# Kernel tuning notes

Measured on AMD Instinct MI355X. Metric: run time of the kernel, lower is better.

The kernel has to match this reference:

```python
import jax, jax.numpy as jnp
import numpy as np
from jax import lax

T = 16384
L = 1024  # num_labels; START = L-2, STOP = L-1
NEG = -10000.0


def setup_inputs() -> dict:
    key = jax.random.key(0)
    k1, k2, k3 = jax.random.split(key, 3)
    pred_logits = jax.random.normal(k1, (T, L), dtype=jnp.float32)
    # gold tags avoid the reserved START (L-2) and STOP (L-1) tags
    ref = jax.random.randint(k2, (T,), 0, L - 2)
    transitions = jax.random.normal(k3, (L, L), dtype=jnp.float32)
    transitions = transitions.at[L - 2, :].set(NEG).at[L - 1, :].set(NEG)
    return {"pred_logits": pred_logits, "ref": ref, "transitions": transitions}


def reference(pred_logits, ref, transitions):
    num_labels = transitions.shape[0]
    START = num_labels - 2
    STOP = num_labels - 1

    # ---- forward algorithm (log-sum-exp recurrence over tags) ----
    init = jnp.full((num_labels,), NEG, dtype=pred_logits.dtype).at[START].set(0.0)

    def step(alpha, feat):
        # new_alpha[j] = logsumexp_i(alpha[i] + transitions[j, i]) + feat[j]
        new_alpha = jax.nn.logsumexp(alpha[None, :] + transitions, axis=1) + feat
        return new_alpha, None

    alpha, _ = lax.scan(step, init, pred_logits)
    forward_score = jax.nn.logsumexp(alpha + transitions[STOP])

    # ---- gold path score ----
    prev = jnp.concatenate([jnp.array([START], dtype=ref.dtype), ref[:-1]])
    trans_score = transitions[ref, prev].sum()
    emit_score = jnp.take_along_axis(pred_logits, ref[:, None], axis=1).sum()
    gold_score = trans_score + emit_score + transitions[STOP, ref[-1]]

    # torch returns shape (1,)
    return (forward_score - gold_score).reshape(1)
```

## Files before the change

kernel.cpp:

```cpp
#include <hip/hip_runtime.h>


#define TT    16384
#define LLAB  1024
#define NEGV  -10000.0
#define BQ    32
#define NCH   512
#define KCH   32
#define NPTY  8
#define AGT   __HIP_MEMORY_SCOPE_AGENT

typedef unsigned long long u64;
typedef unsigned int u32;
typedef unsigned short u16;
typedef _Float16 f16;
typedef _Float16 h2 __attribute__((ext_vector_type(2)));
typedef _Float16 f16x8 __attribute__((ext_vector_type(8)));
typedef float f32x4 __attribute__((ext_vector_type(4)));

__device__ __forceinline__ void pub64(u64* p, u64 v) {
  __hip_atomic_store(p, v, __ATOMIC_RELAXED, AGT);
}
__device__ __forceinline__ u64 ald64(const u64* p) {
  return __hip_atomic_load(p, __ATOMIC_RELAXED, AGT);
}
__device__ __forceinline__ u32 pack2(float a, float b) {
  h2 h = {(f16)a, (f16)b};
  return __builtin_bit_cast(u32, h);
}
__device__ __forceinline__ float f16lo(u32 b) {
  return (float)__builtin_bit_cast(f16, (u16)(b & 0xFFFFu));
}
__device__ __forceinline__ float f16hi(u32 b) {
  return (float)__builtin_bit_cast(f16, (u16)(b >> 16));
}
__device__ __forceinline__ int swz(int c, int w) { return w ^ ((c & 7) << 2); }

__device__ __forceinline__ float max4(u32 a, u32 b) {
  return fmaxf(fmaxf(f16lo(a), f16hi(a)), fmaxf(f16lo(b), f16hi(b)));
}

__global__ __launch_bounds__(256) void crf_gold(const float* __restrict__ pred,
                                                const int* __restrict__ ref,
                                                const float* __restrict__ trans,
                                                float* __restrict__ gold) {
  int t = blockIdx.x * 256 + threadIdx.x;
  int r = ref[t];
  int prev = (t == 0) ? (LLAB - 2) : ref[t - 1];
  float v = trans[(size_t)r * LLAB + prev] + pred[(size_t)t * LLAB + r];
  if (t == TT - 1) v += trans[(size_t)(LLAB - 1) * LLAB + r];
#pragma unroll
  for (int off = 32; off >= 1; off >>= 1) v += __shfl_xor(v, off);
  __shared__ float acc[4];
  if ((threadIdx.x & 63) == 0) acc[threadIdx.x >> 6] = v;
  __syncthreads();
  if (threadIdx.x == 0) atomicAdd(gold, acc[0] + acc[1] + acc[2] + acc[3]);
}

__global__ __launch_bounds__(256) void transpose_k(const float* __restrict__ in,
                                                   float* __restrict__ out) {
  __shared__ float t[32][33];
  int bx = blockIdx.x & 31, by = blockIdx.x >> 5;
  int r0 = by * 32, c0 = bx * 32;
  int lr = threadIdx.x >> 3;
  int lc = threadIdx.x & 7;
  float4 v = *(const float4*)&in[(size_t)(r0 + lr) * LLAB + c0 + 4 * lc];
  t[lr][4 * lc] = v.x; t[lr][4 * lc + 1] = v.y;
  t[lr][4 * lc + 2] = v.z; t[lr][4 * lc + 3] = v.w;
  __syncthreads();
  float4 o = {t[4 * lc][lr], t[4 * lc + 1][lr], t[4 * lc + 2][lr], t[4 * lc + 3][lr]};
  *(float4*)&out[(size_t)(c0 + lr) * LLAB + r0 + 4 * lc] = o;
}

__global__ __launch_bounds__(256, 1) void crf_chunks(
    const float* __restrict__ pred, const float* __restrict__ trans,
    const float* __restrict__ transT, u64* __restrict__ pay,
    u32* __restrict__ fl, float* __restrict__ ybuf,
    float* __restrict__ zbuf, double* __restrict__ tlog) {
  const int tid = threadIdx.x;
  const int wv = tid >> 6, l = tid & 63;
  const int lm = l & 15, lg = l >> 4;
  const int gc = tid >> 3, tp = tid & 7;
  const int b = blockIdx.x;
  const int g = b & 31;
  const int party = b >> 5;
  const bool isFwd = (g < 16);
  const int cbase = (g & 15) * KCH;
  const int c1 = cbase + lm, c2 = cbase + lm + 16;
  const int tb1 = c1 * BQ, tb2 = c2 * BQ;
  const int wb = 128 * party + 32 * wv;

  const float* M = isFwd ? trans : transT;
  f16x8 afrag0[32], afrag1[32];
  {
    const float4* rp0 = (const float4*)&M[(size_t)(wb + lm) * LLAB];
    const float4* rp1 = (const float4*)&M[(size_t)(wb + 16 + lm) * LLAB];
#pragma unroll
    for (int kt = 0; kt < 32; ++kt) {
      float4 a = rp0[8 * kt + 2 * lg], c = rp0[8 * kt + 2 * lg + 1];
      f16x8 f;
      f[0] = (f16)__expf(a.x); f[1] = (f16)__expf(a.y);
      f[2] = (f16)__expf(a.z); f[3] = (f16)__expf(a.w);
      f[4] = (f16)__expf(c.x); f[5] = (f16)__expf(c.y);
      f[6] = (f16)__expf(c.z); f[7] = (f16)__expf(c.w);
      afrag0[kt] = f;
      a = rp1[8 * kt + 2 * lg]; c = rp1[8 * kt + 2 * lg + 1];
      f[0] = (f16)__expf(a.x); f[1] = (f16)__expf(a.y);
      f[2] = (f16)__expf(a.z); f[3] = (f16)__expf(a.w);
      f[4] = (f16)__expf(c.x); f[5] = (f16)__expf(c.y);
      f[6] = (f16)__expf(c.z); f[7] = (f16)__expf(c.w);
      afrag1[kt] = f;
    }
  }

  __shared__ __attribute__((aligned(16))) u32 qs[KCH * 512];
  __shared__ float smax[KCH];

  u64* gp64 = pay + (size_t)g * 16384;
  u32* gfl  = fl + (size_t)g * 512;

  {
    float mm;
    if (isFwd) {
      uint4 ones = {0x3C003C00u, 0x3C003C00u, 0x3C003C00u, 0x3C003C00u};
#pragma unroll
      for (int i = 0; i < 16; ++i)
        *(uint4*)&qs[gc * 512 + swz(gc, 64 * tp + 4 * i)] = ones;
      mm = 1.0f;
    } else {
      int trow = (cbase + gc) * BQ + BQ - 1;
      const float4* pp = (const float4*)&pred[(size_t)trow * LLAB + 128 * tp];
      mm = 0.f;
#pragma unroll
      for (int i = 0; i < 16; ++i) {
        float4 e0 = pp[2 * i], e1 = pp[2 * i + 1];
        float a0 = __expf(e0.x), a1 = __expf(e0.y);
        float a2 = __expf(e0.z), a3 = __expf(e0.w);
        float a4 = __expf(e1.x), a5 = __expf(e1.y);
        float a6 = __expf(e1.z), a7 = __expf(e1.w);
        uint4 w4 = {pack2(a0, a1), pack2(a2, a3), pack2(a4, a5), pack2(a6, a7)};
        *(uint4*)&qs[gc * 512 + swz(gc, 64 * tp + 4 * i)] = w4;
        mm = fmaxf(mm, fmaxf(fmaxf(a0, a1), fmaxf(a2, a3)));
        mm = fmaxf(mm, fmaxf(fmaxf(a4, a5), fmaxf(a6, a7)));
      }
#pragma unroll
      for (int off = 1; off <= 4; off <<= 1) mm = fmaxf(mm, __shfl_xor(mm, off));
    }
    if (tp == 0) smax[gc] = mm;
  }
  __syncthreads();

  float4 fe1a, fe1b, fe2a, fe2b;
  {
    int t1 = isFwd ? tb1 : (tb1 + BQ - 2);
    int t2 = isFwd ? tb2 : (tb2 + BQ - 2);
    fe1a = *(const float4*)&pred[(size_t)t1 * LLAB + wb + 4 * lg];
    fe1b = *(const float4*)&pred[(size_t)t1 * LLAB + wb + 16 + 4 * lg];
    fe2a = *(const float4*)&pred[(size_t)t2 * LLAB + wb + 4 * lg];
    fe2b = *(const float4*)&pred[(size_t)t2 * LLAB + wb + 16 + 4 * lg];
  }

  const float C0 = 13359.727f;
  double up = 1.0;

  for (int s = 0; s < BQ; ++s) {
    const bool lastS = (s == BQ - 1);
    const int ps = s & 1;
    const u32 want = (u32)(s + 1);
    if (tid < KCH) up *= (double)smax[tid];
    const float i1 = 1.0f / (C0 * smax[lm]);
    const float i2 = 1.0f / (C0 * smax[lm + 16]);

    f32x4 a00 = {0.f, 0.f, 0.f, 0.f}, a01 = {0.f, 0.f, 0.f, 0.f};
    f32x4 a10 = {0.f, 0.f, 0.f, 0.f}, a11 = {0.f, 0.f, 0.f, 0.f};
#pragma unroll
    for (int kt = 0; kt < 32; ++kt) {
      f16x8 b1 = __builtin_bit_cast(f16x8,
          *(const uint4*)&qs[lm * 512 + swz(lm, 16 * kt + 4 * lg)]);
      f16x8 b2 = __builtin_bit_cast(f16x8,
          *(const uint4*)&qs[(lm + 16) * 512 + swz(lm + 16, 16 * kt + 4 * lg)]);
      a00 = __builtin_amdgcn_mfma_f32_16x16x32_f16(afrag0[kt], b1, a00, 0, 0, 0);
      a01 = __builtin_amdgcn_mfma_f32_16x16x32_f16(afrag1[kt], b1, a01, 0, 0, 0);
      a10 = __builtin_amdgcn_mfma_f32_16x16x32_f16(afrag0[kt], b2, a10, 0, 0, 0);
      a11 = __builtin_amdgcn_mfma_f32_16x16x32_f16(afrag1[kt], b2, a11, 0, 0, 0);
    }

    float4 n1a = fe1a, n1b = fe1b, n2a = fe2a, n2b = fe2b;
    if (!lastS) {
      int sn = s + 1;
      int t1 = isFwd ? (tb1 + sn) : (tb1 + BQ - 2 - sn);
      int t2 = isFwd ? (tb2 + sn) : (tb2 + BQ - 2 - sn);
      if (t1 < tb1) t1 = tb1;
      if (t2 < tb2) t2 = tb2;
      n1a = *(const float4*)&pred[(size_t)t1 * LLAB + wb + 4 * lg];
      n1b = *(const float4*)&pred[(size_t)t1 * LLAB + wb + 16 + 4 * lg];
      n2a = *(const float4*)&pred[(size_t)t2 * LLAB + wb + 4 * lg];
      n2b = *(const float4*)&pred[(size_t)t2 * LLAB + wb + 16 + 4 * lg];
    }

    const bool fold = isFwd || !lastS;
    float o00[4], o01[4], o10[4], o11[4];
    if (fold) {
      o00[0] = a00[0] * __expf(fe1a.x) * i1; o00[1] = a00[1] * __expf(fe1a.y) * i1;
      o00[2] = a00[2] * __expf(fe1a.z) * i1; o00[3] = a00[3] * __expf(fe1a.w) * i1;
      o01[0] = a01[0] * __expf(fe1b.x) * i1; o01[1] = a01[1] * __expf(fe1b.y) * i1;
      o01[2] = a01[2] * __expf(fe1b.z) * i1; o01[3] = a01[3] * __expf(fe1b.w) * i1;
      o10[0] = a10[0] * __expf(fe2a.x) * i2; o10[1] = a10[1] * __expf(fe2a.y) * i2;
      o10[2] = a10[2] * __expf(fe2a.z) * i2; o10[3] = a10[3] * __expf(fe2a.w) * i2;
      o11[0] = a11[0] * __expf(fe2b.x) * i2; o11[1] = a11[1] * __expf(fe2b.y) * i2;
      o11[2] = a11[2] * __expf(fe2b.z) * i2; o11[3] = a11[3] * __expf(fe2b.w) * i2;
    } else {
#pragma unroll
      for (int r = 0; r < 4; ++r) {
        o00[r] = a00[r] * i1; o01[r] = a01[r] * i1;
        o10[r] = a10[r] * i2; o11[r] = a11[r] * i2;
      }
    }

    if (lastS) {
      float* dst = isFwd ? ybuf : zbuf;
      size_t b1 = (size_t)c1 * LLAB + wb + 4 * lg;
      size_t b2 = (size_t)c2 * LLAB + wb + 4 * lg;
#pragma unroll
      for (int r = 0; r < 4; ++r) {
        dst[b1 + r] = o00[r]; dst[b1 + 16 + r] = o01[r];
        dst[b2 + r] = o10[r]; dst[b2 + 16 + r] = o11[r];
      }
      break;
    }

    {
      u64* op = gp64 + (size_t)ps * 8192 + party * 1024;
      int i64 = lm * 32 + 8 * wv + lg;
      pub64(op + i64,       ((u64)pack2(o00[2], o00[3]) << 32) | pack2(o00[0], o00[1]));
      pub64(op + i64 + 4,   ((u64)pack2(o01[2], o01[3]) << 32) | pack2(o01[0], o01[1]));
      pub64(op + i64 + 512, ((u64)pack2(o10[2], o10[3]) << 32) | pack2(o10[0], o10[1]));
      pub64(op + i64 + 516, ((u64)pack2(o11[2], o11[3]) << 32) | pack2(o11[0], o11[1]));
    }
    __syncthreads();
    if (tid == 0)
      __hip_atomic_store(gfl + ps * 256 + party * 32, want, __ATOMIC_RELAXED, AGT);

    {
      const u32* fp = gfl + ps * 256 + (l & 7) * 32;
      bool done = false;
      do {
        if (!done) done = (__hip_atomic_load(fp, __ATOMIC_RELAXED, AGT) >= want);
      } while (!__all(done));
    }

    {
      u64 gv[8][4];
#pragma unroll
      for (int p2 = 0; p2 < 8; ++p2) {
        const u64* pb = gp64 + (size_t)ps * 8192 + p2 * 1024 + tid * 4;
#pragma unroll
        for (int j = 0; j < 4; ++j) gv[p2][j] = ald64(pb + j);
      }
      float mm = 0.f;
#pragma unroll
      for (int p2 = 0; p2 < 8; ++p2) {
#pragma unroll
        for (int j = 0; j < 4; ++j) {
          u32 lo = (u32)gv[p2][j], hi = (u32)(gv[p2][j] >> 32);
          int W = p2 * 64 + 8 * tp + 2 * j;
          uint2 st = {lo, hi};
          *(uint2*)&qs[gc * 512 + swz(gc, W)] = st;
          mm = fmaxf(mm, max4(lo, hi));
        }
      }
#pragma unroll
      for (int off = 1; off <= 4; off <<= 1) mm = fmaxf(mm, __shfl_xor(mm, off));
      if (tp == 0) smax[gc] = mm;
    }
    __syncthreads();
    fe1a = n1a; fe1b = n1b; fe2a = n2a; fe2b = n2b;
  }

  if (!isFwd && party == 0 && tid < KCH) tlog[cbase + tid] = log(up);
}

__global__ __launch_bounds__(256) void crf_stitch(
    const float* __restrict__ ybuf, const float* __restrict__ zbuf,
    const double* __restrict__ tlog, double* __restrict__ dacc) {
  const int cc = blockIdx.x, tid = threadIdx.x;
  double na = 0.0, sa = 0.0;
  for (int j = tid; j < LLAB; j += 256) {
    double yv = (double)ybuf[(size_t)cc * LLAB + j];
    na += yv;
    double zz = (cc + 1 < NCH) ? (double)zbuf[(size_t)(cc + 1) * LLAB + j] : 1.0;
    sa += zz * yv;
  }
#pragma unroll
  for (int off = 32; off >= 1; off >>= 1) {
    na += __shfl_xor(na, off);
    sa += __shfl_xor(sa, off);
  }
  __shared__ double red[2][4];
  if ((tid & 63) == 0) { red[0][tid >> 6] = na; red[1][tid >> 6] = sa; }
  __syncthreads();
  if (tid == 0) {
    double n = red[0][0] + red[0][1] + red[0][2] + red[0][3];
    double sm = red[1][0] + red[1][1] + red[1][2] + red[1][3];
    const double LC0 = log((double)13359.727f);
    atomicAdd(dacc, log(sm) - log(n) + tlog[cc] + (double)BQ * LC0);
  }
}

__global__ void crf_final(const double* __restrict__ dacc,
                          const float* __restrict__ zbuf,
                          const float* __restrict__ gold,
                          float* __restrict__ out) {
  double s = dacc[0] + log((double)zbuf[LLAB - 2]) + NEGV - (double)gold[0];
  out[0] = (float)s;
}

extern "C" void kernel_launch(void* const* d_in, const int* in_sizes, int n_in,
                              void* d_out, int out_size, void* d_ws, size_t ws_size,
                              hipStream_t stream) {
  const float* pred  = (const float*)d_in[0];
  const int*   ref   = (const int*)d_in[1];
  const float* trans = (const float*)d_in[2];
  float* out = (float*)d_out;

  char* ws = (char*)d_ws;
  double* dacc = (double*)(ws + 0);
  float* gold  = (float*)(ws + 8);
  float* transT = (float*)(ws + 1024);
  size_t off = 1024 + (size_t)LLAB * LLAB * 4;
  u64* pay = (u64*)(ws + off);
  off += (size_t)32 * 2 * NPTY * 1024 * 8;
  u32* fl = (u32*)(ws + off);
  const size_t flbytes = (size_t)32 * 512 * 4;
  off += flbytes;
  float* ybuf = (float*)(ws + off); off += (size_t)NCH * LLAB * 4;
  float* zbuf = (float*)(ws + off); off += (size_t)NCH * LLAB * 4;
  double* tlog = (double*)(ws + off);

  hipMemsetAsync(ws, 0, 256, stream);
  hipMemsetAsync(fl, 0, flbytes, stream);
  transpose_k<<<1024, 256, 0, stream>>>(trans, transT);
  crf_gold<<<64, 256, 0, stream>>>(pred, ref, trans, gold);
  crf_chunks<<<256, 256, 0, stream>>>(pred, trans, transT, pay, fl, ybuf, zbuf, tlog);
  crf_stitch<<<NCH, 256, 0, stream>>>(ybuf, zbuf, tlog, dacc);
  crf_final<<<1, 1, 0, stream>>>(dacc, zbuf, gold, out);
}
```

Measured before the change: 373.2 us.

## Fuse auxiliary kernels into chunk kernel and streamline cross-block exchange

Removes the transpose kernel by loading transposed exp-transitions with strided reads directly in the backward blocks. It folds the gold-score computation into the chunk kernel's tail and merges the final reduction into the stitch kernel via an atomic counter, which also replaces two memsets with one. The per-step exchange now keeps each block's own payload in LDS and skips reloading it, and fetches peers' data with 16-byte system-coherent loads instead of 8-byte atomic loads. The result is fewer launches and less global traffic per step, at the cost of uncoalesced setup reads of the transposed matrix.

```diff
diff --git a/kernel.cpp b/kernel.cpp
--- a/kernel.cpp
+++ b/kernel.cpp
@@ -21,8 +21,11 @@
 __device__ __forceinline__ void pub64(u64* p, u64 v) {
   __hip_atomic_store(p, v, __ATOMIC_RELAXED, AGT);
 }
-__device__ __forceinline__ u64 ald64(const u64* p) {
-  return __hip_atomic_load(p, __ATOMIC_RELAXED, AGT);
+__device__ __forceinline__ uint4 ld16_sc(const u32* p) {
+  uint4 r;
+  asm volatile("global_load_dwordx4 %0, %1, off sc0 sc1"
+               : "=v"(r) : "v"(p) : "memory");
+  return r;
 }
 __device__ __forceinline__ u32 pack2(float a, float b) {
   h2 h = {(f16)a, (f16)b};
@@ -36,51 +39,21 @@
 }
 __device__ __forceinline__ int swz(int c, int w) { return w ^ ((c & 7) << 2); }
 
-__device__ __forceinline__ float max4(u32 a, u32 b) {
-  return fmaxf(fmaxf(f16lo(a), f16hi(a)), fmaxf(f16lo(b), f16hi(b)));
-}
-
-__global__ __launch_bounds__(256) void crf_gold(const float* __restrict__ pred,
-                                                const int* __restrict__ ref,
-                                                const float* __restrict__ trans,
-                                                float* __restrict__ gold) {
-  int t = blockIdx.x * 256 + threadIdx.x;
-  int r = ref[t];
-  int prev = (t == 0) ? (LLAB - 2) : ref[t - 1];
-  float v = trans[(size_t)r * LLAB + prev] + pred[(size_t)t * LLAB + r];
-  if (t == TT - 1) v += trans[(size_t)(LLAB - 1) * LLAB + r];
-#pragma unroll
-  for (int off = 32; off >= 1; off >>= 1) v += __shfl_xor(v, off);
-  __shared__ float acc[4];
-  if ((threadIdx.x & 63) == 0) acc[threadIdx.x >> 6] = v;
-  __syncthreads();
-  if (threadIdx.x == 0) atomicAdd(gold, acc[0] + acc[1] + acc[2] + acc[3]);
-}
-
-__global__ __launch_bounds__(256) void transpose_k(const float* __restrict__ in,
-                                                   float* __restrict__ out) {
-  __shared__ float t[32][33];
-  int bx = blockIdx.x & 31, by = blockIdx.x >> 5;
-  int r0 = by * 32, c0 = bx * 32;
-  int lr = threadIdx.x >> 3;
-  int lc = threadIdx.x & 7;
-  float4 v = *(const float4*)&in[(size_t)(r0 + lr) * LLAB + c0 + 4 * lc];
-  t[lr][4 * lc] = v.x; t[lr][4 * lc + 1] = v.y;
-  t[lr][4 * lc + 2] = v.z; t[lr][4 * lc + 3] = v.w;
-  __syncthreads();
-  float4 o = {t[4 * lc][lr], t[4 * lc + 1][lr], t[4 * lc + 2][lr], t[4 * lc + 3][lr]};
-  *(float4*)&out[(size_t)(c0 + lr) * LLAB + r0 + 4 * lc] = o;
+__device__ __forceinline__ float max8(uint4 v) {
+  float m = fmaxf(fmaxf(f16lo(v.x), f16hi(v.x)), fmaxf(f16lo(v.y), f16hi(v.y)));
+  m = fmaxf(m, fmaxf(f16lo(v.z), f16hi(v.z)));
+  m = fmaxf(m, fmaxf(f16lo(v.w), f16hi(v.w)));
+  return m;
 }
 
 __global__ __launch_bounds__(256, 1) void crf_chunks(
     const float* __restrict__ pred, const float* __restrict__ trans,
-    const float* __restrict__ transT, u64* __restrict__ pay,
-    u32* __restrict__ fl, float* __restrict__ ybuf,
-    float* __restrict__ zbuf, double* __restrict__ tlog) {
+    const int* __restrict__ ref, u32* __restrict__ pay, u32* __restrict__ fl,
+    float* __restrict__ ybuf, float* __restrict__ zbuf,
+    double* __restrict__ tlog, float* __restrict__ gold) {
   const int tid = threadIdx.x;
   const int wv = tid >> 6, l = tid & 63;
   const int lm = l & 15, lg = l >> 4;
-  const int gc = tid >> 3, tp = tid & 7;
   const int b = blockIdx.x;
   const int g = b & 31;
   const int party = b >> 5;
@@ -90,11 +63,10 @@
   const int tb1 = c1 * BQ, tb2 = c2 * BQ;
   const int wb = 128 * party + 32 * wv;
 
-  const float* M = isFwd ? trans : transT;
   f16x8 afrag0[32], afrag1[32];
-  {
-    const float4* rp0 = (const float4*)&M[(size_t)(wb + lm) * LLAB];
-    const float4* rp1 = (const float4*)&M[(size_t)(wb + 16 + lm) * LLAB];
+  if (isFwd) {
+    const float4* rp0 = (const float4*)&trans[(size_t)(wb + lm) * LLAB];
+    const float4* rp1 = (const float4*)&trans[(size_t)(wb + 16 + lm) * LLAB];
 #pragma unroll
     for (int kt = 0; kt < 32; ++kt) {
       float4 a = rp0[8 * kt + 2 * lg], c = rp0[8 * kt + 2 * lg + 1];
@@ -111,15 +83,29 @@
       f[6] = (f16)__expf(c.z); f[7] = (f16)__expf(c.w);
       afrag1[kt] = f;
     }
+  } else {
+    const int c0 = wb + lm, cc1 = wb + 16 + lm;
+#pragma unroll
+    for (int kt = 0; kt < 32; ++kt) {
+      f16x8 f0, f1;
+#pragma unroll
+      for (int j = 0; j < 8; ++j) {
+        int k = 32 * kt + 8 * lg + j;
+        f0[j] = (f16)__expf(trans[(size_t)k * LLAB + c0]);
+        f1[j] = (f16)__expf(trans[(size_t)k * LLAB + cc1]);
+      }
+      afrag0[kt] = f0; afrag1[kt] = f1;
+    }
   }
 
   __shared__ __attribute__((aligned(16))) u32 qs[KCH * 512];
   __shared__ float smax[KCH];
 
-  u64* gp64 = pay + (size_t)g * 16384;
-  u32* gfl  = fl + (size_t)g * 512;
+  u32* gpay = pay + (size_t)g * 32768;
+  u32* gfl  = fl + g * 512;
 
   {
+    const int gc = tid >> 3, tp = tid & 7;
     float mm;
     if (isFwd) {
       uint4 ones = {0x3C003C00u, 0x3C003C00u, 0x3C003C00u, 0x3C003C00u};
@@ -219,27 +205,41 @@
 
     if (lastS) {
       float* dst = isFwd ? ybuf : zbuf;
-      size_t b1 = (size_t)c1 * LLAB + wb + 4 * lg;
-      size_t b2 = (size_t)c2 * LLAB + wb + 4 * lg;
+      size_t bb1 = (size_t)c1 * LLAB + wb + 4 * lg;
+      size_t bb2 = (size_t)c2 * LLAB + wb + 4 * lg;
 #pragma unroll
       for (int r = 0; r < 4; ++r) {
-        dst[b1 + r] = o00[r]; dst[b1 + 16 + r] = o01[r];
-        dst[b2 + r] = o10[r]; dst[b2 + 16 + r] = o11[r];
+        dst[bb1 + r] = o00[r]; dst[bb1 + 16 + r] = o01[r];
+        dst[bb2 + r] = o10[r]; dst[bb2 + 16 + r] = o11[r];
       }
       break;
     }
 
+    const u32 q00 = pack2(o00[0], o00[1]), q01 = pack2(o00[2], o00[3]);
+    const u32 q02 = pack2(o01[0], o01[1]), q03 = pack2(o01[2], o01[3]);
+    const u32 q10 = pack2(o10[0], o10[1]), q11 = pack2(o10[2], o10[3]);
+    const u32 q12 = pack2(o11[0], o11[1]), q13 = pack2(o11[2], o11[3]);
     {
-      u64* op = gp64 + (size_t)ps * 8192 + party * 1024;
+      u64* op = (u64*)(gpay + (size_t)ps * 16384 + party * 2048);
       int i64 = lm * 32 + 8 * wv + lg;
-      pub64(op + i64,       ((u64)pack2(o00[2], o00[3]) << 32) | pack2(o00[0], o00[1]));
-      pub64(op + i64 + 4,   ((u64)pack2(o01[2], o01[3]) << 32) | pack2(o01[0], o01[1]));
-      pub64(op + i64 + 512, ((u64)pack2(o10[2], o10[3]) << 32) | pack2(o10[0], o10[1]));
-      pub64(op + i64 + 516, ((u64)pack2(o11[2], o11[3]) << 32) | pack2(o11[0], o11[1]));
+      pub64(op + i64,       ((u64)q01 << 32) | q00);
+      pub64(op + i64 + 4,   ((u64)q03 << 32) | q02);
+      pub64(op + i64 + 512, ((u64)q11 << 32) | q10);
+      pub64(op + i64 + 516, ((u64)q13 << 32) | q12);
     }
     __syncthreads();
     if (tid == 0)
       __hip_atomic_store(gfl + ps * 256 + party * 32, want, __ATOMIC_RELAXED, AGT);
+
+    {
+      int w = 16 * wv + 2 * lg;
+      uint2 s0 = {q00, q01}, s1 = {q02, q03}, s2 = {q10, q11}, s3 = {q12, q13};
+      *(uint2*)&qs[lm * 512 + swz(lm, party * 64 + w)] = s0;
+      *(uint2*)&qs[lm * 512 + swz(lm, party * 64 + w + 8)] = s1;
+      *(uint2*)&qs[(lm + 16) * 512 + swz(lm + 16, party * 64 + w)] = s2;
+      *(uint2*)&qs[(lm + 16) * 512 + swz(lm + 16, party * 64 + w + 8)] = s3;
+    }
+    __syncthreads();
 
     {
       const u32* fp = gfl + ps * 256 + (l & 7) * 32;
@@ -250,69 +250,96 @@
     }
 
     {
-      u64 gv[8][4];
+      const u32* pb = gpay + (size_t)ps * 16384;
+      const int c = tid >> 3, wbase = 8 * (tid & 7);
+      uint4 gv[16];
 #pragma unroll
       for (int p2 = 0; p2 < 8; ++p2) {
-        const u64* pb = gp64 + (size_t)ps * 8192 + p2 * 1024 + tid * 4;
-#pragma unroll
-        for (int j = 0; j < 4; ++j) gv[p2][j] = ald64(pb + j);
-      }
+        if (p2 != party) {
+          gv[2 * p2]     = ld16_sc(pb + p2 * 2048 + tid * 8);
+          gv[2 * p2 + 1] = ld16_sc(pb + p2 * 2048 + tid * 8 + 4);
+        }
+      }
+      asm volatile("s_waitcnt vmcnt(0)" ::: "memory");
+      __builtin_amdgcn_sched_barrier(0);
       float mm = 0.f;
 #pragma unroll
       for (int p2 = 0; p2 < 8; ++p2) {
-#pragma unroll
-        for (int j = 0; j < 4; ++j) {
-          u32 lo = (u32)gv[p2][j], hi = (u32)(gv[p2][j] >> 32);
-          int W = p2 * 64 + 8 * tp + 2 * j;
-          uint2 st = {lo, hi};
-          *(uint2*)&qs[gc * 512 + swz(gc, W)] = st;
-          mm = fmaxf(mm, max4(lo, hi));
+        uint4 va, vb;
+        if (p2 == party) {
+          va = *(const uint4*)&qs[c * 512 + swz(c, p2 * 64 + wbase)];
+          vb = *(const uint4*)&qs[c * 512 + swz(c, p2 * 64 + wbase + 4)];
+        } else {
+          va = gv[2 * p2]; vb = gv[2 * p2 + 1];
+          *(uint4*)&qs[c * 512 + swz(c, p2 * 64 + wbase)] = va;
+          *(uint4*)&qs[c * 512 + swz(c, p2 * 64 + wbase + 4)] = vb;
         }
+        mm = fmaxf(mm, fmaxf(max8(va), max8(vb)));
       }
 #pragma unroll
       for (int off = 1; off <= 4; off <<= 1) mm = fmaxf(mm, __shfl_xor(mm, off));
-      if (tp == 0) smax[gc] = mm;
+      if ((tid & 7) == 0) smax[c] = mm;
     }
     __syncthreads();
     fe1a = n1a; fe1b = n1b; fe2a = n2a; fe2b = n2b;
   }
 
   if (!isFwd && party == 0 && tid < KCH) tlog[cbase + tid] = log(up);
+
+  if (tid < 64) {
+    int t = b * 64 + tid;
+    int r = ref[t];
+    int prev = (t == 0) ? (LLAB - 2) : ref[t - 1];
+    float v = trans[(size_t)r * LLAB + prev] + pred[(size_t)t * LLAB + r];
+    if (t == TT - 1) v += trans[(size_t)(LLAB - 1) * LLAB + r];
+#pragma unroll
+    for (int off = 32; off >= 1; off >>= 1) v += __shfl_xor(v, off);
+    if (tid == 0) atomicAdd(gold, v);
+  }
 }
 
 __global__ __launch_bounds__(256) void crf_stitch(
     const float* __restrict__ ybuf, const float* __restrict__ zbuf,
-    const double* __restrict__ tlog, double* __restrict__ dacc) {
-  const int cc = blockIdx.x, tid = threadIdx.x;
-  double na = 0.0, sa = 0.0;
-  for (int j = tid; j < LLAB; j += 256) {
-    double yv = (double)ybuf[(size_t)cc * LLAB + j];
-    na += yv;
-    double zz = (cc + 1 < NCH) ? (double)zbuf[(size_t)(cc + 1) * LLAB + j] : 1.0;
-    sa += zz * yv;
-  }
-#pragma unroll
-  for (int off = 32; off >= 1; off >>= 1) {
-    na += __shfl_xor(na, off);
-    sa += __shfl_xor(sa, off);
-  }
+    const double* __restrict__ tlog, const float* __restrict__ gold,
+    double* __restrict__ dacc, u32* __restrict__ cnt, float* __restrict__ out) {
+  const int tid = threadIdx.x;
   __shared__ double red[2][4];
-  if ((tid & 63) == 0) { red[0][tid >> 6] = na; red[1][tid >> 6] = sa; }
-  __syncthreads();
+  double local = 0.0;
+  const double LC0 = log((double)13359.727f);
+#pragma unroll
+  for (int i = 0; i < 4; ++i) {
+    const int cc = blockIdx.x * 4 + i;
+    double na = 0.0, sa = 0.0;
+    for (int j = tid; j < LLAB; j += 256) {
+      double yv = (double)ybuf[(size_t)cc * LLAB + j];
+      na += yv;
+      double zz = (cc + 1 < NCH) ? (double)zbuf[(size_t)(cc + 1) * LLAB + j] : 1.0;
+      sa += zz * yv;
+    }
+#pragma unroll
+    for (int off = 32; off >= 1; off >>= 1) {
+      na += __shfl_xor(na, off);
+      sa += __shfl_xor(sa, off);
+    }
+    if ((tid & 63) == 0) { red[0][tid >> 6] = na; red[1][tid >> 6] = sa; }
+    __syncthreads();
+    if (tid == 0) {
+      double n = red[0][0] + red[0][1] + red[0][2] + red[0][3];
+      double sm = red[1][0] + red[1][1] + red[1][2] + red[1][3];
+      local += log(sm) - log(n) + tlog[cc] + (double)BQ * LC0;
+    }
+    __syncthreads();
+  }
   if (tid == 0) {
-    double n = red[0][0] + red[0][1] + red[0][2] + red[0][3];
-    double sm = red[1][0] + red[1][1] + red[1][2] + red[1][3];
-    const double LC0 = log((double)13359.727f);
-    atomicAdd(dacc, log(sm) - log(n) + tlog[cc] + (double)BQ * LC0);
-  }
-}
-
-__global__ void crf_final(const double* __restrict__ dacc,
-                          const float* __restrict__ zbuf,
-                          const float* __restrict__ gold,
-                          float* __restrict__ out) {
-  double s = dacc[0] + log((double)zbuf[LLAB - 2]) + NEGV - (double)gold[0];
-  out[0] = (float)s;
+    atomicAdd(dacc, local);
+    __threadfence();
+    u32 old = atomicAdd(cnt, 1u);
+    if (old == 127u) {
+      __threadfence();
+      double s = __hip_atomic_load(dacc, __ATOMIC_RELAXED, AGT);
+      out[0] = (float)(s + log((double)zbuf[LLAB - 2]) + NEGV - (double)gold[0]);
+    }
+  }
 }
 
 extern "C" void kernel_launch(void* const* d_in, const int* in_sizes, int n_in,
@@ -326,22 +353,16 @@
   char* ws = (char*)d_ws;
   double* dacc = (double*)(ws + 0);
   float* gold  = (float*)(ws + 8);
-  float* transT = (float*)(ws + 1024);
-  size_t off = 1024 + (size_t)LLAB * LLAB * 4;
-  u64* pay = (u64*)(ws + off);
-  off += (size_t)32 * 2 * NPTY * 1024 * 8;
-  u32* fl = (u32*)(ws + off);
-  const size_t flbytes = (size_t)32 * 512 * 4;
-  off += flbytes;
+  u32* cnt     = (u32*)(ws + 16);
+  u32* fl      = (u32*)(ws + 256);
+  u32* pay     = (u32*)(ws + 66560);
+  size_t off = 66560 + (size_t)32 * 32768 * 4;
   float* ybuf = (float*)(ws + off); off += (size_t)NCH * LLAB * 4;
   float* zbuf = (float*)(ws + off); off += (size_t)NCH * LLAB * 4;
   double* tlog = (double*)(ws + off);
 
-  hipMemsetAsync(ws, 0, 256, stream);
-  hipMemsetAsync(fl, 0, flbytes, stream);
-  transpose_k<<<1024, 256, 0, stream>>>(trans, transT);
-  crf_gold<<<64, 256, 0, stream>>>(pred, ref, trans, gold);
-  crf_chunks<<<256, 256, 0, stream>>>(pred, trans, transT, pay, fl, ybuf, zbuf, tlog);
-  crf_stitch<<<NCH, 256, 0, stream>>>(ybuf, zbuf, tlog, dacc);
-  crf_final<<<1, 1, 0, stream>>>(dacc, zbuf, gold, out);
-}
+  hipMemsetAsync(ws, 0, 66560, stream);
+  crf_chunks<<<256, 256, 0, stream>>>(pred, trans, ref, pay, fl, ybuf, zbuf,
+                                      tlog, gold);
+  crf_stitch<<<128, 256, 0, stream>>>(ybuf, zbuf, tlog, gold, dacc, cnt, out);
+}
```

Result: faster. 359.1 us (-3.8%).
